# Kernel tuning notes

Measured on AMD Instinct MI355X. Metric: run time of the kernel, lower is better.

The kernel has to match this reference:

```python
import jax, jax.numpy as jnp
import numpy as np

B, H, W, C, NH, WS, DEPTH = 32, 56, 56, 192, 6, 7, 2
SHIFTS = (0, WS // 2)
N = WS * WS
NW = (H // WS) * (W // WS)
HD = C // NH
SCALE = HD ** -0.5


def _rel_index():
    coords = np.stack(np.meshgrid(np.arange(WS), np.arange(WS), indexing='ij')).reshape(2, -1)
    rel = (coords[:, :, None] - coords[:, None, :]).transpose(1, 2, 0)
    rel[..., 0] += WS - 1
    rel[..., 1] += WS - 1
    rel[..., 0] *= 2 * WS - 1
    return jnp.asarray(rel.sum(-1))  # (N, N) int

REL_IDX = _rel_index()


def _attn_mask():
    # BasicLayer.creat_mask for the shifted block (shift = WS//2)
    img = np.zeros((H, W))
    sl = (slice(0, -WS), slice(-WS, -SHIFTS[1]), slice(-SHIFTS[1], None))
    cnt = 0
    for hs in sl:
        for ws_ in sl:
            img[hs, ws_] = cnt
            cnt += 1
    mw = img.reshape(H // WS, WS, W // WS, WS).transpose(0, 2, 1, 3).reshape(-1, N)
    d = mw[:, None, :] - mw[:, :, None]  # unsqueeze(1) - unsqueeze(2)
    return jnp.asarray(np.where(d != 0, -100.0, 0.0).astype(np.float32))  # (NW, N, N)

ATTN_MASK = _attn_mask()


def _ln(x, w, b):
    mu = x.mean(-1, keepdims=True)
    var = ((x - mu) ** 2).mean(-1, keepdims=True)
    return (x - mu) * jax.lax.rsqrt(var + 1e-5) * w + b


def _block(x, p, shift):
    Bn, L, Cc = x.shape
    shortcut = x
    h = _ln(x, p['n1w'], p['n1b']).reshape(Bn, H, W, Cc)
    if shift > 0:
        h = jnp.roll(h, (-shift, -shift), axis=(1, 2))
    # window_partition -> (Bn*NW, N, C)
    h = h.reshape(Bn, H // WS, WS, W // WS, WS, Cc).transpose(0, 1, 3, 2, 4, 5).reshape(-1, N, Cc)
    qkv = (h @ p['qkvw'].T + p['qkvb']).reshape(-1, N, 3, NH, HD).transpose(2, 0, 3, 1, 4)
    q, k, v = qkv[0] * SCALE, qkv[1], qkv[2]  # (Bw, NH, N, HD)
    attn = jnp.einsum('bhnd,bhmd->bhnm', q, k)
    bias = p['rpb'][REL_IDX].transpose(2, 0, 1)  # (NH, N, N)
    attn = attn + bias[None]
    if shift > 0:
        attn = attn.reshape(Bn, NW, NH, N, N) + ATTN_MASK[None, :, None]
        attn = attn.reshape(-1, NH, N, N)
    attn = jax.nn.softmax(attn, axis=-1)
    h = jnp.einsum('bhnm,bhmd->bhnd', attn, v).transpose(0, 2, 1, 3).reshape(-1, N, Cc)
    h = h @ p['projw'].T + p['projb']
    # window_reverse
    h = h.reshape(Bn, H // WS, W // WS, WS, WS, Cc).transpose(0, 1, 3, 2, 4, 5).reshape(Bn, H, W, Cc)
    if shift > 0:
        # NOTE: source rolls back by window_size (not shift_size); replicated faithfully
        h = jnp.roll(h, (WS, WS), axis=(1, 2))
    x = shortcut + h.reshape(Bn, L, Cc)
    m = _ln(x, p['n2w'], p['n2b'])
    m = jax.nn.gelu(m @ p['f1w'].T + p['f1b'], approximate=False) @ p['f2w'].T + p['f2b']
    return x + m


def setup_inputs() -> dict:
    key = jax.random.key(0)
    ks = jax.random.split(key, 15)
    r = lambda k, s, sc: jax.random.normal(k, s, dtype=jnp.float32) * sc
    return {
        'x': r(ks[0], (B, H * W, C), 1.0),
        'n1w': 1.0 + r(ks[1], (DEPTH, C), 0.01),
        'n1b': r(ks[2], (DEPTH, C), 0.01),
        'qkvw': r(ks[3], (DEPTH, 3 * C, C), 0.05),
        'qkvb': r(ks[4], (DEPTH, 3 * C), 0.01),
        'rpb': r(ks[5], (DEPTH, (2 * WS - 1) ** 2, NH), 0.02),
        'projw': r(ks[6], (DEPTH, C, C), 0.05),
        'projb': r(ks[7], (DEPTH, C), 0.01),
        'n2w': 1.0 + r(ks[8], (DEPTH, C), 0.01),
        'n2b': r(ks[9], (DEPTH, C), 0.01),
        'f1w': r(ks[10], (DEPTH, 4 * C, C), 0.05),
        'f1b': r(ks[11], (DEPTH, 4 * C), 0.01),
        'f2w': r(ks[12], (DEPTH, C, 4 * C), 0.05),
        'f2b': r(ks[13], (DEPTH, C), 0.01),
    }


def reference(x, n1w, n1b, qkvw, qkvb, rpb, projw, projb, n2w, n2b, f1w, f1b, f2w, f2b):
    for i in range(DEPTH):
        p = {'n1w': n1w[i], 'n1b': n1b[i], 'qkvw': qkvw[i], 'qkvb': qkvb[i],
             'rpb': rpb[i], 'projw': projw[i], 'projb': projb[i],
             'n2w': n2w[i], 'n2b': n2b[i], 'f1w': f1w[i], 'f1b': f1b[i],
             'f2w': f2w[i], 'f2b': f2b[i]}
        x = _block(x, p, SHIFTS[i])
    return x
```

## Files before the change

kernel.cpp:

```cpp
#include <hip/hip_runtime.h>
#include <hip/hip_bf16.h>
#include <math.h>

typedef __hip_bfloat16 bf16;

#define BB    32
#define HH    56
#define WWI   56
#define CC    192
#define NHH   6
#define WSS   7
#define NN    49
#define NWIN  64
#define HDD   32
#define LL    (HH*WWI)
#define ROWS  (BB*NWIN*NN)
#define TOT   ((size_t)ROWS*CC)
#define SCALEQ 0.17677669529663687f

#define OFF_N1W   0
#define OFF_N1B   384
#define OFF_QKVW  768
#define OFF_QKVB  221952
#define OFF_RPB   223104
#define OFF_PROJW 225132
#define OFF_PROJB 298860
#define OFF_N2W   299244
#define OFF_N2B   299628
#define OFF_F1W   300012
#define OFF_F1B   594924
#define OFF_F2W   596460
#define OFF_F2B   891372

typedef __bf16 bf16x8v __attribute__((ext_vector_type(8)));
typedef float  f32x4   __attribute__((ext_vector_type(4)));

__device__ __forceinline__ float tof(bf16 v){ return __bfloat162float(v); }
__device__ __forceinline__ bf16  tob(float v){ return __float2bfloat16(v); }
__device__ __forceinline__ float xload(const float* p){ return *p; }
__device__ __forceinline__ float xload(const bf16*  p){ return tof(*p); }
__device__ __forceinline__ void  xstore(float* p, float v){ *p = v; }
__device__ __forceinline__ void  xstore(bf16*  p, float v){ *p = tob(v); }

__device__ __forceinline__ bf16x8v ldfrag(const bf16* p){
    return *(const bf16x8v*)p;
}
__device__ __forceinline__ unsigned short bfbits(float v){
    bf16 b = tob(v);
    return __builtin_bit_cast(unsigned short, b);
}
__device__ __forceinline__ bf16 mkbf(unsigned short u){
    return __builtin_bit_cast(bf16, u);
}

template<typename XT>
__device__ __forceinline__ float ldx(const void* p, size_t i, int dynf){
    if (dynf < 0) return xload(((const XT*)p) + i);
    return dynf ? tof(((const bf16*)p)[i]) : ((const float*)p)[i];
}

__device__ __forceinline__ float fast_gelu(float x){
    float u = fabsf(x) * 0.70710678118f;
    float t = __builtin_amdgcn_rcpf(1.f + 0.3275911f*u);
    float p = t*(0.254829592f + t*(-0.284496736f + t*(1.421413741f +
              t*(-1.453152027f + t*1.061405429f))));
    float e = __expf(-u*u);
    float erfu = 1.f - p*e;
    float s = copysignf(erfu, x);
    return 0.5f*x*(1.f + s);
}

__global__ void k_detect(const unsigned short* __restrict__ w, int* __restrict__ flag){
    if (blockIdx.x == 0 && threadIdx.x == 0){
        int cnt = 0;
        for (int k = 0; k < 16; ++k){
            unsigned short u = w[2*k];
            if (u >= 0x3E00 && u <= 0x4100) ++cnt;
        }
        *flag = (cnt >= 8) ? 1 : 0;
    }
}

__global__ void k_canon(const void* __restrict__ src, bf16* __restrict__ dst,
                        int n, const int* __restrict__ flag){
    int i = blockIdx.x * blockDim.x + threadIdx.x;
    if (i >= n) return;
    if (*flag) dst[i] = ((const bf16*)src)[i];
    else       dst[i] = tob(((const float*)src)[i]);
}

template<typename XT>
__global__ __launch_bounds__(256) void k_out(const XT* __restrict__ X,
        void* __restrict__ out, const int* __restrict__ flag){
    size_t i = ((size_t)blockIdx.x * 256 + threadIdx.x) * 8;
    if (i >= TOT) return;
    float v[8];
    if constexpr (sizeof(XT) == 4){
        f32x4 a = *(const f32x4*)((const float*)X + i);
        f32x4 b = *(const f32x4*)((const float*)X + i + 4);
        #pragma unroll
        for (int e = 0; e < 4; ++e){ v[e] = a[e]; v[4+e] = b[e]; }
    } else {
        bf16x8v a = ldfrag((const bf16*)X + i);
        #pragma unroll
        for (int e = 0; e < 8; ++e) v[e] = tof(mkbf(__builtin_bit_cast(unsigned short, a[e])));
    }
    if (*flag){
        bf16x8v o;
        #pragma unroll
        for (int e = 0; e < 8; ++e) o[e] = __builtin_bit_cast(__bf16, bfbits(v[e]));
        *(bf16x8v*)((bf16*)out + i) = o;
    } else {
        f32x4 o0, o1;
        #pragma unroll
        for (int e = 0; e < 4; ++e){ o0[e] = v[e]; o1[e] = v[4+e]; }
        *(f32x4*)((float*)out + i)     = o0;
        *(f32x4*)((float*)out + i + 4) = o1;
    }
}

template<typename XT>
__global__ __launch_bounds__(256) void k_ln_part(const void* __restrict__ src,
        int dynsrc, const int* __restrict__ flag,
        const bf16* __restrict__ w, const bf16* __restrict__ bsh,
        bf16* __restrict__ Hwin, int shift){
    int dynf = dynsrc ? flag[0] : -1;
    int wv = threadIdx.x >> 6, lane = threadIdx.x & 63;
    int row = blockIdx.x*4 + wv;
    int b   = row / (NWIN*NN);
    int win = (row / NN) % NWIN;
    int n   = row % NN;
    int wh = win >> 3, ww = win & 7;
    int iy = n / WSS, ix = n % WSS;
    int sy = (wh*WSS + iy + shift) % HH;
    int sx = (ww*WSS + ix + shift) % WWI;
    size_t base = ((size_t)(b*LL + sy*WWI + sx))*CC;
    float v0 = ldx<XT>(src, base + lane,       dynf);
    float v1 = ldx<XT>(src, base + lane + 64,  dynf);
    float v2 = ldx<XT>(src, base + lane + 128, dynf);
    float sm  = v0+v1+v2;
    float sm2 = v0*v0+v1*v1+v2*v2;
    #pragma unroll
    for (int st = 1; st < 64; st <<= 1){
        sm  += __shfl_xor(sm,  st);
        sm2 += __shfl_xor(sm2, st);
    }
    float mu  = sm * (1.f/CC);
    float inv = rsqrtf(sm2*(1.f/CC) - mu*mu + 1e-5f);
    bf16* dst = Hwin + (size_t)row*CC;
    dst[lane]     = tob((v0-mu)*inv*tof(w[lane])     + tof(bsh[lane]));
    dst[lane+64]  = tob((v1-mu)*inv*tof(w[lane+64])  + tof(bsh[lane+64]));
    dst[lane+128] = tob((v2-mu)*inv*tof(w[lane+128]) + tof(bsh[lane+128]));
}

__device__ __forceinline__ int mt0(int i){ return (i < 3) ? i*16 : 33; }

__global__ __launch_bounds__(512, 4) void k_attn(const bf16* __restrict__ Hwin,
        const bf16* __restrict__ qkvw, const bf16* __restrict__ qkvb,
        const bf16* __restrict__ rpb, bf16* __restrict__ AOut, int masked){
    __shared__ bf16 smem[31104];
    bf16* qls = smem;
    bf16* kls = smem + 9408;
    bf16* vT  = smem + 18816;
    bf16* Pls = smem;

    int t = threadIdx.x;
    int win  = blockIdx.x;
    int winl = win & (NWIN-1);
    int wh = winl >> 3, ww = winl & 7;
    int wv = t >> 6, lane = t & 63;
    int li16 = lane & 15, quad = lane >> 4;

    for (int idx = t; idx < 192*15; idx += 512){
        int d = idx / 15, tokp = 49 + idx % 15;
        vT[d*64 + (tokp ^ ((d&7)<<3))] = tob(0.f);
    }

    {
        int p = wv & 1, c = wv >> 1;
        int m0a = mt0(2*p), m0b = mt0(2*p+1);
        const bf16* hg = Hwin + (size_t)win*NN*CC;
        bf16x8v afa[6], afb[6];
        #pragma unroll
        for (int kc = 0; kc < 6; ++kc){
            afa[kc] = ldfrag(hg + (m0a+li16)*CC + kc*32 + quad*8);
            afb[kc] = ldfrag(hg + (m0b+li16)*CC + kc*32 + quad*8);
        }
        #pragma unroll 3
        for (int j = 0; j < 9; ++j){
            int nt = c + 4*j;
            int col = nt*16 + li16;
            f32x4 acc0 = {0.f,0.f,0.f,0.f}, acc1 = {0.f,0.f,0.f,0.f};
            #pragma unroll
            for (int kc = 0; kc < 6; ++kc){
                bf16x8v bfr = ldfrag(qkvw + (size_t)col*CC + kc*32 + quad*8);
                acc0 = __builtin_amdgcn_mfma_f32_16x16x32_bf16(afa[kc], bfr, acc0, 0, 0, 0);
                acc1 = __builtin_amdgcn_mfma_f32_16x16x32_bf16(afb[kc], bfr, acc1, 0, 0, 0);
            }
            float bias = tof(qkvb[col]);
            int m  = col / CC;
            int cm = col - m*CC;
            #pragma unroll
            for (int r = 0; r < 4; ++r){
                int rowA = m0a + quad*4 + r;
                int rowB = m0b + quad*4 + r;
                float v0 = acc0[r] + bias, v1 = acc1[r] + bias;
                if (m == 0){
                    qls[rowA*CC + (cm ^ ((rowA&7)<<3))] = tob(v0*SCALEQ);
                    qls[rowB*CC + (cm ^ ((rowB&7)<<3))] = tob(v1*SCALEQ);
                } else if (m == 1){
                    kls[rowA*CC + (cm ^ ((rowA&7)<<3))] = tob(v0);
                    kls[rowB*CC + (cm ^ ((rowB&7)<<3))] = tob(v1);
                } else {
                    vT[cm*64 + (rowA ^ ((cm&7)<<3))] = tob(v0);
                    vT[cm*64 + (rowB ^ ((cm&7)<<3))] = tob(v1);
                }
            }
        }
    }
    __syncthreads();

    unsigned int pk[3][8];
    #pragma unroll
    for (int j = 0; j < 3; ++j){
        int id = wv + 8*j;
        int mt = id & 3, h = id >> 2;
        int m0 = mt0(mt);
        int rowq = m0 + li16;
        bf16x8v afr = ldfrag(qls + rowq*CC + ((h*32 + quad*8) ^ ((rowq&7)<<3)));
        f32x4 s[4];
        #pragma unroll
        for (int nt = 0; nt < 4; ++nt){
            int rowk = nt*16 + li16;
            bf16x8v bfr = ldfrag(kls + rowk*CC + ((h*32 + quad*8) ^ ((rowk&7)<<3)));
            f32x4 z = {0.f,0.f,0.f,0.f};
            s[nt] = __builtin_amdgcn_mfma_f32_16x16x32_bf16(afr, bfr, z, 0, 0, 0);
        }
        #pragma unroll
        for (int nt = 0; nt < 4; ++nt){
            int jj = nt*16 + li16;
            int valid = (jj < NN);
            int jc = valid ? jj : 48;
            int yj = (jc*37) >> 8, xj = jc - 7*yj;
            int lj = 0;
            if (masked){
                int ayj = wh*WSS + yj, axj = ww*WSS + xj;
                lj = ((ayj<49)?0:(ayj<53)?1:2)*3 + ((axj<49)?0:(axj<53)?1:2);
            }
            #pragma unroll
            for (int r = 0; r < 4; ++r){
                int i = m0 + quad*4 + r;
                int yi = (i*37) >> 8, xi = i - 7*yi;
                int ridx = (yi - yj + 6)*13 + (xi - xj + 6);
                float v = s[nt][r] + tof(rpb[ridx*NHH + h]);
                if (masked){
                    int ayi = wh*WSS + yi, axi = ww*WSS + xi;
                    int li = ((ayi<49)?0:(ayi<53)?1:2)*3 + ((axi<49)?0:(axi<53)?1:2);
                    if (li != lj) v -= 100.f;
                }
                s[nt][r] = valid ? v : -1e30f;
            }
        }
        float mx[4], sm[4];
        #pragma unroll
        for (int r = 0; r < 4; ++r)
            mx[r] = fmaxf(fmaxf(s[0][r], s[1][r]), fmaxf(s[2][r], s[3][r]));
        #pragma unroll
        for (int st = 1; st < 16; st <<= 1){
            #pragma unroll
            for (int r = 0; r < 4; ++r) mx[r] = fmaxf(mx[r], __shfl_xor(mx[r], st));
        }
        #pragma unroll
        for (int nt = 0; nt < 4; ++nt){
            #pragma unroll
            for (int r = 0; r < 4; ++r) s[nt][r] = __expf(s[nt][r] - mx[r]);
        }
        #pragma unroll
        for (int r = 0; r < 4; ++r) sm[r] = (s[0][r]+s[1][r]) + (s[2][r]+s[3][r]);
        #pragma unroll
        for (int st = 1; st < 16; st <<= 1){
            #pragma unroll
            for (int r = 0; r < 4; ++r) sm[r] += __shfl_xor(sm[r], st);
        }
        #pragma unroll
        for (int r = 0; r < 4; ++r) sm[r] = 1.f / sm[r];
        #pragma unroll
        for (int nt = 0; nt < 4; ++nt){
            #pragma unroll
            for (int rr = 0; rr < 2; ++rr){
                unsigned int u0 = bfbits(s[nt][2*rr]   * sm[2*rr]);
                unsigned int u1 = bfbits(s[nt][2*rr+1] * sm[2*rr+1]);
                pk[j][nt*2+rr] = (u1 << 16) | u0;
            }
        }
    }
    __syncthreads();

    #pragma unroll
    for (int j = 0; j < 3; ++j){
        int id = wv + 8*j;
        int m0 = mt0(id & 3), h = id >> 2;
        #pragma unroll
        for (int nt = 0; nt < 4; ++nt){
            int jj = nt*16 + li16;
            #pragma unroll
            for (int rr = 0; rr < 2; ++rr){
                unsigned int u = pk[j][nt*2+rr];
                int tok0 = m0 + quad*4 + 2*rr;
                int tok1 = tok0 + 1;
                Pls[(h*NN + tok0)*64 + (jj ^ ((tok0&7)<<3))] = mkbf((unsigned short)(u & 0xffff));
                Pls[(h*NN + tok1)*64 + (jj ^ ((tok1&7)<<3))] = mkbf((unsigned short)(u >> 16));
            }
        }
    }
    __syncthreads();

    {
        int mt = wv & 3, nto = wv >> 2;
        int m0 = mt0(mt), n0 = nto*16;
        #pragma unroll
        for (int h = 0; h < NHH; ++h){
            f32x4 acc = {0.f,0.f,0.f,0.f};
            #pragma unroll
            for (int kc = 0; kc < 2; ++kc){
                int rowp = m0 + li16;
                bf16x8v afr = ldfrag(Pls + (h*NN + rowp)*64 + ((kc*32 + quad*8) ^ ((rowp&7)<<3)));
                int rowv = h*HDD + n0 + li16;
                bf16x8v bfr = ldfrag(vT + rowv*64 + ((kc*32 + quad*8) ^ ((rowv&7)<<3)));
                acc = __builtin_amdgcn_mfma_f32_16x16x32_bf16(afr, bfr, acc, 0, 0, 0);
            }
            #pragma unroll
            for (int r = 0; r < 4; ++r){
                int tok = m0 + quad*4 + r;
                AOut[(size_t)win*NN*CC + tok*CC + h*HDD + n0 + li16] = tob(acc[r]);
            }
        }
    }
}

#define AS_STRIDE 200
template<typename XT>
__global__ __launch_bounds__(256) void k_proj_res(const bf16* __restrict__ AOut,
        const bf16* __restrict__ pw, const bf16* __restrict__ pb,
        const void* rsrc, int dynsrc, const int* __restrict__ flag,
        XT* __restrict__ X, int shift){
    __shared__ bf16 as[32*AS_STRIDE];
    int fl = dynsrc ? flag[0] : 0;
    int t = threadIdx.x;
    int row0 = blockIdx.x * 32;
    for (int idx = t; idx < 32*24; idx += 256){
        int r = idx / 24, c8 = idx % 24;
        *(bf16x8v*)(as + r*AS_STRIDE + c8*8) = ldfrag(AOut + (size_t)(row0 + r)*CC + c8*8);
    }
    __syncthreads();
    int wv = t >> 6, lane = t & 63;
    int li16 = lane & 15, quad = lane >> 4;
    int roll = (shift > 0) ? WSS : 0;
    for (int nt = 0; nt < 3; ++nt){
        int n0 = wv*48 + nt*16;
        int col = n0 + li16;
        bf16x8v bfr[6];
        #pragma unroll
        for (int kc = 0; kc < 6; ++kc)
            bfr[kc] = ldfrag(pw + (size_t)col*CC + kc*32 + quad*8);
        float bias = tof(pb[col]);
        for (int mt = 0; mt < 2; ++mt){
            int m0 = mt*16;
            f32x4 acc = {0.f,0.f,0.f,0.f};
            #pragma unroll
            for (int kc = 0; kc < 6; ++kc){
                bf16x8v afr = ldfrag(as + (m0 + li16)*AS_STRIDE + kc*32 + quad*8);
                acc = __builtin_amdgcn_mfma_f32_16x16x32_bf16(afr, bfr[kc], acc, 0, 0, 0);
            }
            #pragma unroll
            for (int r = 0; r < 4; ++r){
                int grow = row0 + m0 + quad*4 + r;
                int b   = grow / (NWIN*NN);
                int rem = grow % (NWIN*NN);
                int win = rem / NN;
                int n   = rem % NN;
                int wh = win >> 3, ww = win & 7;
                int iy = n / WSS, ix = n % WSS;
                int y = (wh*WSS + iy + roll) % HH;
                int x = (ww*WSS + ix + roll) % WWI;
                size_t idx = ((size_t)(b*LL + y*WWI + x))*CC + col;
                float res;
                if (dynsrc)
                    res = fl ? tof(((const bf16*)rsrc)[idx])
                             : ((const float*)rsrc)[idx];
                else
                    res = xload(&X[idx]);
                xstore(&X[idx], res + acc[r] + bias);
            }
        }
    }
}

template<typename XT>
__global__ __launch_bounds__(256, 3) void k_mlp(XT* __restrict__ X,
        const bf16* __restrict__ n2w, const bf16* __restrict__ n2b,
        const bf16* __restrict__ w1, const bf16* __restrict__ b1,
        const bf16* __restrict__ w2, const bf16* __restrict__ b2){
    __shared__ bf16 xin[64*192];
    __shared__ bf16 h1p[64*192];
    int t = threadIdx.x;
    int wv = t >> 6, lane = t & 63;
    int li16 = lane & 15, quad = lane >> 4;
    size_t row0 = (size_t)blockIdx.x * 64;

    {
        float nw0 = tof(n2w[lane]), nw1 = tof(n2w[lane+64]), nw2 = tof(n2w[lane+128]);
        float nb0 = tof(n2b[lane]), nb1 = tof(n2b[lane+64]), nb2 = tof(n2b[lane+128]);
        #pragma unroll 4
        for (int i = 0; i < 16; ++i){
            int r = wv*16 + i;
            const XT* xr = X + (row0 + r)*CC;
            float v0 = xload(&xr[lane]);
            float v1 = xload(&xr[lane+64]);
            float v2 = xload(&xr[lane+128]);
            float sm  = v0+v1+v2;
            float sm2 = v0*v0+v1*v1+v2*v2;
            #pragma unroll
            for (int st = 1; st < 64; st <<= 1){
                sm  += __shfl_xor(sm,  st);
                sm2 += __shfl_xor(sm2, st);
            }
            float mu  = sm * (1.f/CC);
            float inv = rsqrtf(sm2*(1.f/CC) - mu*mu + 1e-5f);
            int swz = (r&7)<<3;
            bf16* xrow = xin + r*192;
            xrow[lane        ^ swz] = tob((v0-mu)*inv*nw0 + nb0);
            xrow[(lane+64)   ^ swz] = tob((v1-mu)*inv*nw1 + nb1);
            xrow[(lane+128)  ^ swz] = tob((v2-mu)*inv*nw2 + nb2);
        }
    }
    __syncthreads();

    int sw = (li16 & 7) << 3;
    f32x4 acc2[3][4];
    #pragma unroll
    for (int j = 0; j < 3; ++j)
        #pragma unroll
        for (int m = 0; m < 4; ++m)
            acc2[j][m] = (f32x4){0.f,0.f,0.f,0.f};

    #pragma unroll 1
    for (int pass = 0; pass < 4; ++pass){
        #pragma unroll
        for (int j = 0; j < 3; ++j){
            int cl  = (wv*3 + j)*16 + li16;
            int col = pass*192 + cl;
            f32x4 a1[4];
            #pragma unroll
            for (int m = 0; m < 4; ++m) a1[m] = (f32x4){0.f,0.f,0.f,0.f};
            #pragma unroll
            for (int kc = 0; kc < 6; ++kc){
                bf16x8v bfr = ldfrag(w1 + (size_t)col*CC + kc*32 + quad*8);
                #pragma unroll
                for (int m = 0; m < 4; ++m){
                    bf16x8v af = ldfrag(xin + (m*16 + li16)*192 + ((kc*32 + quad*8) ^ sw));
                    a1[m] = __builtin_amdgcn_mfma_f32_16x16x32_bf16(af, bfr, a1[m], 0, 0, 0);
                }
            }
            float bb = tof(b1[col]);
            #pragma unroll
            for (int m = 0; m < 4; ++m){
                #pragma unroll
                for (int r = 0; r < 4; ++r){
                    int row = m*16 + quad*4 + r;
                    h1p[row*192 + (cl ^ ((row&7)<<3))] = tob(fast_gelu(a1[m][r] + bb));
                }
            }
        }
        __syncthreads();
        #pragma unroll
        for (int kc = 0; kc < 6; ++kc){
            bf16x8v af[4];
            #pragma unroll
            for (int m = 0; m < 4; ++m)
                af[m] = ldfrag(h1p + (m*16 + li16)*192 + ((kc*32 + quad*8) ^ sw));
            int kg = pass*6 + kc;
            #pragma unroll
            for (int j = 0; j < 3; ++j){
                int col = wv*48 + j*16 + li16;
                bf16x8v bfr = ldfrag(w2 + (size_t)col*768 + kg*32 + quad*8);
                #pragma unroll
                for (int m = 0; m < 4; ++m)
                    acc2[j][m] = __builtin_amdgcn_mfma_f32_16x16x32_bf16(af[m], bfr, acc2[j][m], 0, 0, 0);
            }
        }
        __syncthreads();
    }

    #pragma unroll
    for (int j = 0; j < 3; ++j){
        int col = wv*48 + j*16 + li16;
        float bias = tof(b2[col]);
        #pragma unroll
        for (int m = 0; m < 4; ++m){
            #pragma unroll
            for (int r = 0; r < 4; ++r){
                size_t idx = (row0 + m*16 + quad*4 + r)*CC + col;
                xstore(&X[idx], xload(&X[idx]) + acc2[j][m][r] + bias);
            }
        }
    }
}

template<typename XT>
static void run_pipeline(const bf16* wb, const void* xin0, int* flag,
                         XT* X, bf16* Hwin, bf16* AOut, void* out,
                         hipStream_t stream){
    for (int i = 0; i < 2; ++i){
        int shift = i ? (WSS/2) : 0;
        const void* src = (i == 0) ? xin0 : (const void*)X;
        int dynsrc = (i == 0) ? 1 : 0;
        k_ln_part<XT><<<ROWS/4, 256, 0, stream>>>(src, dynsrc, flag,
                wb+OFF_N1W + i*CC, wb+OFF_N1B + i*CC, Hwin, shift);
        k_attn<<<BB*NWIN, 512, 0, stream>>>(Hwin,
                wb+OFF_QKVW + (size_t)i*3*CC*CC, wb+OFF_QKVB + (size_t)i*3*CC,
                wb+OFF_RPB + (size_t)i*169*NHH, AOut, i);
        k_proj_res<XT><<<ROWS/32, 256, 0, stream>>>(AOut,
                wb+OFF_PROJW + (size_t)i*CC*CC, wb+OFF_PROJB + i*CC,
                src, dynsrc, flag, X, shift);
        k_mlp<XT><<<ROWS/64, 256, 0, stream>>>(X,
                wb+OFF_N2W + i*CC, wb+OFF_N2B + i*CC,
                wb+OFF_F1W + (size_t)i*4*CC*CC, wb+OFF_F1B + (size_t)i*4*CC,
                wb+OFF_F2W + (size_t)i*CC*4*CC, wb+OFF_F2B + i*CC);
    }
    k_out<XT><<<(int)(TOT/2048), 256, 0, stream>>>(X, out, flag);
}

extern "C" void kernel_launch(void* const* d_in, const int* in_sizes, int n_in,
                              void* d_out, int out_size, void* d_ws, size_t ws_size,
                              hipStream_t stream){
    char* p = (char*)d_ws;
    int*  flag = (int*)p;
    bf16* wb   = (bf16*)(p + 16);
    char* q    = p + 16 + (2u<<20);

    k_detect<<<1, 64, 0, stream>>>((const unsigned short*)d_in[1], flag);

    static const int widx[13] = {1,2,3,4,5,6,7,8,9,10,11,12,13};
    static const int woff[13] = {OFF_N1W,OFF_N1B,OFF_QKVW,OFF_QKVB,OFF_RPB,
                                 OFF_PROJW,OFF_PROJB,OFF_N2W,OFF_N2B,
                                 OFF_F1W,OFF_F1B,OFF_F2W,OFF_F2B};
    static const int wsz[13]  = {384,384,221184,1152,2028,73728,384,384,384,
                                 294912,1536,294912,384};
    for (int k = 0; k < 13; ++k)
        k_canon<<<(wsz[k]+255)/256, 256, 0, stream>>>(d_in[widx[k]], wb+woff[k],
                                                      wsz[k], flag);

    size_t needF32 = 16 + (2u<<20) + TOT*4 + TOT*2 + TOT*2;
    if (ws_size >= needF32){
        float* X   = (float*)q;       q += TOT*4;
        bf16* Hwin = (bf16*)q;        q += TOT*2;
        bf16* AOut = (bf16*)q;
        run_pipeline<float>(wb, d_in[0], flag, X, Hwin, AOut, d_out, stream);
    } else {
        bf16* X    = (bf16*)q;        q += TOT*2;
        bf16* Hwin = (bf16*)q;        q += TOT*2;
        bf16* AOut = (bf16*)q;
        run_pipeline<bf16>(wb, d_in[0], flag, X, Hwin, AOut, d_out, stream);
    }
}
```

Measured before the change: 1.090 ms.

## Fuse output projection and residual add into the window attention kernel

Moves the projection GEMM, bias add and residual update (including window-reverse and roll indexing) into the attention kernel. The per-window attention output is staged in shared memory, so it no longer has to be written to and re-read from a global AOut buffer, and one kernel launch per block goes away. In exchange, each attention workgroup now loads the full 192x192 projection weight, does more work, and may use more registers, which can lower occupancy.

```diff
diff --git a/kernel.cpp b/kernel.cpp
--- a/kernel.cpp
+++ b/kernel.cpp
@@ -155,15 +155,22 @@
 
 __device__ __forceinline__ int mt0(int i){ return (i < 3) ? i*16 : 33; }
 
+#define OL_ST 200
+template<typename XT>
 __global__ __launch_bounds__(512, 4) void k_attn(const bf16* __restrict__ Hwin,
         const bf16* __restrict__ qkvw, const bf16* __restrict__ qkvb,
-        const bf16* __restrict__ rpb, bf16* __restrict__ AOut, int masked){
+        const bf16* __restrict__ rpb,
+        const bf16* __restrict__ pw, const bf16* __restrict__ pb,
+        const void* rsrc, int dynsrc, const int* __restrict__ flag,
+        XT* __restrict__ X, int masked){
     __shared__ bf16 smem[31104];
     bf16* qls = smem;
     bf16* kls = smem + 9408;
     bf16* vT  = smem + 18816;
     bf16* Pls = smem;
-
+    bf16* OLs = smem;
+
+    int fl = dynsrc ? flag[0] : 0;
     int t = threadIdx.x;
     int win  = blockIdx.x;
     int winl = win & (NWIN-1);
@@ -315,6 +322,7 @@
     }
     __syncthreads();
 
+    f32x4 oacc[6];
     {
         int mt = wv & 3, nto = wv >> 2;
         int m0 = mt0(mt), n0 = nto*16;
@@ -329,68 +337,62 @@
                 bf16x8v bfr = ldfrag(vT + rowv*64 + ((kc*32 + quad*8) ^ ((rowv&7)<<3)));
                 acc = __builtin_amdgcn_mfma_f32_16x16x32_bf16(afr, bfr, acc, 0, 0, 0);
             }
+            oacc[h] = acc;
+        }
+    }
+    __syncthreads();
+
+    {
+        int mt = wv & 3, nto = wv >> 2;
+        int m0 = mt0(mt), n0 = nto*16;
+        #pragma unroll
+        for (int h = 0; h < NHH; ++h){
             #pragma unroll
             for (int r = 0; r < 4; ++r){
                 int tok = m0 + quad*4 + r;
-                AOut[(size_t)win*NN*CC + tok*CC + h*HDD + n0 + li16] = tob(acc[r]);
-            }
-        }
-    }
-}
-
-#define AS_STRIDE 200
-template<typename XT>
-__global__ __launch_bounds__(256) void k_proj_res(const bf16* __restrict__ AOut,
-        const bf16* __restrict__ pw, const bf16* __restrict__ pb,
-        const void* rsrc, int dynsrc, const int* __restrict__ flag,
-        XT* __restrict__ X, int shift){
-    __shared__ bf16 as[32*AS_STRIDE];
-    int fl = dynsrc ? flag[0] : 0;
-    int t = threadIdx.x;
-    int row0 = blockIdx.x * 32;
-    for (int idx = t; idx < 32*24; idx += 256){
-        int r = idx / 24, c8 = idx % 24;
-        *(bf16x8v*)(as + r*AS_STRIDE + c8*8) = ldfrag(AOut + (size_t)(row0 + r)*CC + c8*8);
+                OLs[tok*OL_ST + h*HDD + n0 + li16] = tob(oacc[h][r]);
+            }
+        }
     }
     __syncthreads();
-    int wv = t >> 6, lane = t & 63;
-    int li16 = lane & 15, quad = lane >> 4;
-    int roll = (shift > 0) ? WSS : 0;
-    for (int nt = 0; nt < 3; ++nt){
-        int n0 = wv*48 + nt*16;
-        int col = n0 + li16;
-        bf16x8v bfr[6];
-        #pragma unroll
-        for (int kc = 0; kc < 6; ++kc)
-            bfr[kc] = ldfrag(pw + (size_t)col*CC + kc*32 + quad*8);
-        float bias = tof(pb[col]);
-        for (int mt = 0; mt < 2; ++mt){
-            int m0 = mt*16;
-            f32x4 acc = {0.f,0.f,0.f,0.f};
-            #pragma unroll
-            for (int kc = 0; kc < 6; ++kc){
-                bf16x8v afr = ldfrag(as + (m0 + li16)*AS_STRIDE + kc*32 + quad*8);
-                acc = __builtin_amdgcn_mfma_f32_16x16x32_bf16(afr, bfr[kc], acc, 0, 0, 0);
-            }
-            #pragma unroll
-            for (int r = 0; r < 4; ++r){
-                int grow = row0 + m0 + quad*4 + r;
-                int b   = grow / (NWIN*NN);
-                int rem = grow % (NWIN*NN);
-                int win = rem / NN;
-                int n   = rem % NN;
-                int wh = win >> 3, ww = win & 7;
-                int iy = n / WSS, ix = n % WSS;
-                int y = (wh*WSS + iy + roll) % HH;
-                int x = (ww*WSS + ix + roll) % WWI;
-                size_t idx = ((size_t)(b*LL + y*WWI + x))*CC + col;
-                float res;
-                if (dynsrc)
-                    res = fl ? tof(((const bf16*)rsrc)[idx])
-                             : ((const float*)rsrc)[idx];
-                else
-                    res = xload(&X[idx]);
-                xstore(&X[idx], res + acc[r] + bias);
+
+    {
+        int b = win >> 6;
+        int roll = masked ? WSS : 0;
+        int mthalf = wv >> 2, ntg = wv & 3;
+        #pragma unroll
+        for (int j = 0; j < 3; ++j){
+            int col = (ntg*3 + j)*16 + li16;
+            bf16x8v bfr[6];
+            #pragma unroll
+            for (int kc = 0; kc < 6; ++kc)
+                bfr[kc] = ldfrag(pw + (size_t)col*CC + kc*32 + quad*8);
+            float bias = tof(pb[col]);
+            #pragma unroll
+            for (int mtl = 0; mtl < 2; ++mtl){
+                int m0 = mt0(mthalf*2 + mtl);
+                f32x4 acc = {0.f,0.f,0.f,0.f};
+                #pragma unroll
+                for (int kc = 0; kc < 6; ++kc){
+                    bf16x8v afr = ldfrag(OLs + (m0 + li16)*OL_ST + kc*32 + quad*8);
+                    acc = __builtin_amdgcn_mfma_f32_16x16x32_bf16(afr, bfr[kc], acc, 0, 0, 0);
+                }
+                #pragma unroll
+                for (int r = 0; r < 4; ++r){
+                    int tok = m0 + quad*4 + r;
+                    if (m0 == 33 && tok != 48) continue;
+                    int iy = (tok*37) >> 8, ix = tok - 7*iy;
+                    int y = (wh*WSS + iy + roll) % HH;
+                    int x = (ww*WSS + ix + roll) % WWI;
+                    size_t idx = ((size_t)(b*LL + y*WWI + x))*CC + col;
+                    float res;
+                    if (dynsrc)
+                        res = fl ? tof(((const bf16*)rsrc)[idx])
+                                 : ((const float*)rsrc)[idx];
+                    else
+                        res = xload(&X[idx]);
+                    xstore(&X[idx], res + acc[r] + bias);
+                }
             }
         }
     }
@@ -509,7 +511,7 @@
 
 template<typename XT>
 static void run_pipeline(const bf16* wb, const void* xin0, int* flag,
-                         XT* X, bf16* Hwin, bf16* AOut, void* out,
+                         XT* X, bf16* Hwin, void* out,
                          hipStream_t stream){
     for (int i = 0; i < 2; ++i){
         int shift = i ? (WSS/2) : 0;
@@ -517,12 +519,11 @@
         int dynsrc = (i == 0) ? 1 : 0;
         k_ln_part<XT><<<ROWS/4, 256, 0, stream>>>(src, dynsrc, flag,
                 wb+OFF_N1W + i*CC, wb+OFF_N1B + i*CC, Hwin, shift);
-        k_attn<<<BB*NWIN, 512, 0, stream>>>(Hwin,
+        k_attn<XT><<<BB*NWIN, 512, 0, stream>>>(Hwin,
                 wb+OFF_QKVW + (size_t)i*3*CC*CC, wb+OFF_QKVB + (size_t)i*3*CC,
-                wb+OFF_RPB + (size_t)i*169*NHH, AOut, i);
-        k_proj_res<XT><<<ROWS/32, 256, 0, stream>>>(AOut,
+                wb+OFF_RPB + (size_t)i*169*NHH,
                 wb+OFF_PROJW + (size_t)i*CC*CC, wb+OFF_PROJB + i*CC,
-                src, dynsrc, flag, X, shift);
+                src, dynsrc, flag, X, i);
         k_mlp<XT><<<ROWS/64, 256, 0, stream>>>(X,
                 wb+OFF_N2W + i*CC, wb+OFF_N2B + i*CC,
                 wb+OFF_F1W + (size_t)i*4*CC*CC, wb+OFF_F1B + (size_t)i*4*CC,
@@ -551,16 +552,14 @@
         k_canon<<<(wsz[k]+255)/256, 256, 0, stream>>>(d_in[widx[k]], wb+woff[k],
                                                       wsz[k], flag);
 
-    size_t needF32 = 16 + (2u<<20) + TOT*4 + TOT*2 + TOT*2;
+    size_t needF32 = 16 + (2u<<20) + TOT*4 + TOT*2;
     if (ws_size >= needF32){
         float* X   = (float*)q;       q += TOT*4;
-        bf16* Hwin = (bf16*)q;        q += TOT*2;
-        bf16* AOut = (bf16*)q;
-        run_pipeline<float>(wb, d_in[0], flag, X, Hwin, AOut, d_out, stream);
+        bf16* Hwin = (bf16*)q;
+        run_pipeline<float>(wb, d_in[0], flag, X, Hwin, d_out, stream);
     } else {
         bf16* X    = (bf16*)q;        q += TOT*2;
-        bf16* Hwin = (bf16*)q;        q += TOT*2;
-        bf16* AOut = (bf16*)q;
-        run_pipeline<bf16>(wb, d_in[0], flag, X, Hwin, AOut, d_out, stream);
-    }
-}
+        bf16* Hwin = (bf16*)q;
+        run_pipeline<bf16>(wb, d_in[0], flag, X, Hwin, d_out, stream);
+    }
+}
```

New measurement: 1.090 ms. Within noise of the previous version (-0.1%).
